# Performance work log

Hardware: AMD Instinct MI355X
Metric: run time of the kernel (lower is better)

The kernel has to match this reference:

```python
import jax, jax.numpy as jnp
import numpy as np

DIM = 1024
HIDDEN = 4096
NNZ = 262144
X_SHAPE = (2, 256, DIM)


def setup_inputs() -> dict:
    key = jax.random.key(0)
    ks = jax.random.split(key, 13)
    return {
        "x": jax.random.normal(ks[0], X_SHAPE, dtype=jnp.float32),
        "up_row": jax.random.randint(ks[1], (NNZ,), 0, HIDDEN),
        "up_col": jax.random.randint(ks[2], (NNZ,), 0, DIM),
        "up_val": jax.random.normal(ks[3], (NNZ,), dtype=jnp.float32),
        "up_bias": jax.random.normal(ks[4], (HIDDEN,), dtype=jnp.float32),
        "gate_row": jax.random.randint(ks[5], (NNZ,), 0, HIDDEN),
        "gate_col": jax.random.randint(ks[6], (NNZ,), 0, DIM),
        "gate_val": jax.random.normal(ks[7], (NNZ,), dtype=jnp.float32),
        "gate_bias": jax.random.normal(ks[8], (HIDDEN,), dtype=jnp.float32),
        "down_row": jax.random.randint(ks[9], (NNZ,), 0, DIM),
        "down_col": jax.random.randint(ks[10], (NNZ,), 0, HIDDEN),
        "down_val": jax.random.normal(ks[11], (NNZ,), dtype=jnp.float32),
        "down_bias": jax.random.normal(ks[12], (DIM,), dtype=jnp.float32),
    }


def _sparse_linear(x2d, row, col, val, bias, out_features):
    # x2d: [T, in_features]; COO: row -> out_features, col -> in_features
    weighted = x2d[:, col] * val  # [T, nnz], same expanded form as torch gather*mul
    # scatter_add over rows == segment_sum over the nnz axis
    out = jax.ops.segment_sum(weighted.T, row, num_segments=out_features).T  # [T, out]
    return out + bias


def reference(x, up_row, up_col, up_val, up_bias,
              gate_row, gate_col, gate_val, gate_bias,
              down_row, down_col, down_val, down_bias):
    in_shape = x.shape
    x2d = x.reshape(-1, DIM)  # [T, dim]
    up = _sparse_linear(x2d, up_row, up_col, up_val, up_bias, HIDDEN)
    gate = _sparse_linear(x2d, gate_row, gate_col, gate_val, gate_bias, HIDDEN)
    hidden = jax.nn.silu(up) * gate  # [T, hidden]
    down = _sparse_linear(hidden, down_row, down_col, down_val, down_bias, DIM)
    return (x2d + down).reshape(in_shape)
```

## Files before the change

### kernel.cpp

```cpp
#include <hip/hip_runtime.h>
#include <hip/hip_bf16.h>
#include <stdint.h>


#define DIM_    1024
#define HIDDEN_ 4096
#define NNZ_    262144
#define TTOK_   512
#define PADL_   12

typedef __attribute__((ext_vector_type(8))) short short8;
typedef __attribute__((ext_vector_type(4))) float float4v;

__device__ inline unsigned short f2bf(float f) {
    union { float f; unsigned int u; } c; c.f = f;
    unsigned int u = c.u;
    unsigned int r = u + 0x7fffu + ((u >> 16) & 1u);
    return (unsigned short)(r >> 16);
}

__device__ inline void async16(const unsigned short* g, unsigned short* l) {
    __builtin_amdgcn_global_load_lds(
        (const __attribute__((address_space(1))) unsigned int*)g,
        (__attribute__((address_space(3))) unsigned int*)l, 16, 0, 0);
}

#define PIPE_BAR(N)                                                         \
    __builtin_amdgcn_sched_barrier(0);                                      \
    asm volatile("s_waitcnt vmcnt(" #N ") lgkmcnt(0)" ::: "memory");        \
    __builtin_amdgcn_s_barrier();                                           \
    __builtin_amdgcn_sched_barrier(0);

#define XC_ ((TTOK_ * DIM_) / 4)

__global__ __launch_bounds__(256) void bin_prep_kernel(
    const int* __restrict__ ur, const int* __restrict__ uc, const float* __restrict__ uv,
    const int* __restrict__ gr, const int* __restrict__ gc, const float* __restrict__ gv,
    const int* __restrict__ dr, const int* __restrict__ dc, const float* __restrict__ dv,
    const float* __restrict__ x, const float* __restrict__ down_bias,
    unsigned int* __restrict__ bands, int* __restrict__ cnt,
    int* __restrict__ goc, uint2* __restrict__ gof,
    unsigned short* __restrict__ xb, float* __restrict__ out) {
    const int b = blockIdx.x;
    const int t = threadIdx.x;
    if (b >= 768) {
        const unsigned int u0 = (b - 768) * 1024 + t * 4;
        #pragma unroll
        for (int q = 0; q < 4; ++q) {
            const unsigned int id = u0 + q;
            if (id < XC_) {
                float4 v = ((const float4*)x)[id];
                ushort4 o;
                o.x = f2bf(v.x); o.y = f2bf(v.y); o.z = f2bf(v.z); o.w = f2bf(v.w);
                ((ushort4*)xb)[id] = o;
            } else {
                const unsigned int i = id - XC_;
                float4 v = ((const float4*)x)[i];
                const int d = (i * 4) & (DIM_ - 1);
                const float4 bb = *(const float4*)(down_bias + d);
                float4 o;
                o.x = v.x + bb.x; o.y = v.y + bb.y; o.z = v.z + bb.z; o.w = v.w + bb.w;
                ((float4*)out)[i] = o;
            }
        }
        return;
    }
    __shared__ unsigned int stage[256][PADL_];
    __shared__ int lcount[256];
    const int mat = b >> 8;
    const int chunk = b & 255;
    const int*   rs = (mat == 0) ? ur : (mat == 1) ? gr : dr;
    const int*   cs = (mat == 0) ? uc : (mat == 1) ? gc : dc;
    const float* vs = (mat == 0) ? uv : (mat == 1) ? gv : dv;
    const int shift = (mat == 2) ? 2 : 4;
    const int rmask = (mat == 2) ? 3 : 15;
    lcount[t] = 0;
    __syncthreads();

    const int base = chunk * 1024 + t * 4;
    int4   r4 = *(const int4*)(rs + base);
    int4   c4 = *(const int4*)(cs + base);
    float4 v4 = *(const float4*)(vs + base);
    int   rr[4] = {r4.x, r4.y, r4.z, r4.w};
    int   cc[4] = {c4.x, c4.y, c4.z, c4.w};
    float vv[4] = {v4.x, v4.y, v4.z, v4.w};
    #pragma unroll
    for (int j = 0; j < 4; ++j) {
        const int band = rr[j] >> shift;
        const unsigned int e = ((unsigned int)(rr[j] & rmask) << 28)
                             | ((unsigned int)cc[j] << 16)
                             | (unsigned int)f2bf(vv[j]);
        const int pos = atomicAdd(&lcount[band], 1);
        if (pos < PADL_) {
            stage[band][pos] = e;
        } else {
            const int op = atomicAdd(&goc[mat], 1);
            gof[mat * 4096 + op] = make_uint2((unsigned int)band, e);
        }
    }
    __syncthreads();
    unsigned int* seg = bands + ((unsigned int)(mat * 256 + t) * 256 + chunk) * PADL_;
    const uint4* sp = (const uint4*)&stage[t][0];
    *(uint4*)(seg)     = sp[0];
    *(uint4*)(seg + 4) = sp[1];
    *(uint4*)(seg + 8) = sp[2];
    cnt[(mat * 256 + t) * 256 + chunk] = lcount[t];
}

__global__ __launch_bounds__(512) void build_ug_kernel(
    const unsigned int* __restrict__ bands,
    const int* __restrict__ cnt,
    const int* __restrict__ goc, const uint2* __restrict__ gof,
    unsigned short* __restrict__ WUP,
    unsigned short* __restrict__ WGATE) {
    __shared__ float acc[8 * 1024];
    __shared__ int lcnt[256];
    const int b = blockIdx.x;
    const int t = threadIdx.x;
    const int mat = b >> 9;
    const int rem = b & 511;
    const int band = rem >> 1;
    const int hb = rem & 1;
    unsigned short* out = (mat ? WGATE : WUP) + (band * 16 + hb * 8) * 1024;
    const unsigned int rbase = hb * 8;

    for (int k = 0; k < 4; ++k)
        *(float4*)&acc[(k * 512 + t) * 4] = make_float4(0.f, 0.f, 0.f, 0.f);
    if (t < 256) lcnt[t] = cnt[(mat * 256 + band) * 256 + t];
    __syncthreads();

    const int chunk = t & 255;
    const int half = t >> 8;
    const unsigned int* seg = bands + ((unsigned int)(mat * 256 + band) * 256 + chunk) * PADL_;
    const int c = lcnt[chunk];

    if (half == 0) {
        uint4 q[3];
        const uint4* sp = (const uint4*)seg;
        #pragma unroll
        for (int i = 0; i < 3; ++i) q[i] = sp[i];
        const unsigned int* qq = (const unsigned int*)q;
        #pragma unroll
        for (int j = 0; j < PADL_; ++j) {
            const unsigned int e = qq[j];
            const unsigned int r2 = (e >> 28) - rbase;
            if (j < c && r2 < 8u)
                atomicAdd(&acc[r2 * 1024 + ((e >> 16) & 0xFFFu)],
                          __uint_as_float(e << 16));
        }
    } else {
        const int oc = goc[mat] < 4096 ? goc[mat] : 4096;
        for (int i = chunk; i < oc; i += 256) {
            uint2 oe = gof[mat * 4096 + i];
            if ((int)oe.x == band) {
                const unsigned int e = oe.y;
                const unsigned int r2 = (e >> 28) - rbase;
                if (r2 < 8u)
                    atomicAdd(&acc[r2 * 1024 + ((e >> 16) & 0xFFFu)],
                              __uint_as_float(e << 16));
            }
        }
    }
    __syncthreads();

    for (int k = 0; k < 4; ++k) {
        const int cc = (k * 512 + t) * 4;
        ushort4 o;
        o.x = f2bf(acc[cc]);     o.y = f2bf(acc[cc + 1]);
        o.z = f2bf(acc[cc + 2]); o.w = f2bf(acc[cc + 3]);
        *(ushort4*)(out + cc) = o;
    }
}

#define STAGE_UG(buf, k0)                                      \
    async16(gA + (k0),  sA_  + (buf) * 2048 + t * 8);          \
    async16(gBu + (k0), sBu_ + (buf) * 2048 + t * 8);          \
    async16(gBg + (k0), sBg_ + (buf) * 2048 + t * 8);

#define COMPUTE_UG(buf)                                                        \
    {                                                                          \
        const int kb = (buf) * 2048 + lkq * 8;                                 \
        short8 a[2], bu[2], bg[2];                                             \
        _Pragma("unroll")                                                      \
        for (int im = 0; im < 2; ++im)                                         \
            a[im] = *(const short8*)&sA_[kb + (wm + im * 16 + lr) * 32];       \
        _Pragma("unroll")                                                      \
        for (int in = 0; in < 2; ++in) {                                       \
            bu[in] = *(const short8*)&sBu_[kb + (wn + in * 16 + lr) * 32];     \
            bg[in] = *(const short8*)&sBg_[kb + (wn + in * 16 + lr) * 32];     \
        }                                                                      \
        _Pragma("unroll")                                                      \
        for (int im = 0; im < 2; ++im)                                         \
            _Pragma("unroll")                                                  \
            for (int in = 0; in < 2; ++in) {                                   \
                au[im][in] = __builtin_amdgcn_mfma_f32_16x16x32_bf16(          \
                    a[im], bu[in], au[im][in], 0, 0, 0);                       \
                ag[im][in] = __builtin_amdgcn_mfma_f32_16x16x32_bf16(          \
                    a[im], bg[in], ag[im][in], 0, 0, 0);                       \
            }                                                                  \
    }

__global__ __launch_bounds__(256) void fused_upgate_builddown_kernel(
    const unsigned short* __restrict__ xb,
    const unsigned short* __restrict__ wup,
    const unsigned short* __restrict__ wgate,
    const float* __restrict__ up_bias,
    const float* __restrict__ gate_bias,
    unsigned short* __restrict__ hid,
    const unsigned int* __restrict__ bands,
    const int* __restrict__ cnt,
    const int* __restrict__ goc, const uint2* __restrict__ gof,
    unsigned short* __restrict__ WDOWN) {
    __shared__ __align__(16) unsigned short smem_us[9 * 2048];
    const int b = blockIdx.x;
    const int t = threadIdx.x;

    if (b >= 512) {
        float* acc = (float*)smem_us;
        int*   lcnt = (int*)(smem_us + 16384);
        const int rem = b - 512;
        const int band = rem >> 1;
        const int hb = rem & 1;
        const unsigned int rbase = hb * 2;
        unsigned short* out = WDOWN + (band * 4 + hb * 2) * 4096;

        #pragma unroll
        for (int k = 0; k < 8; ++k)
            *(float4*)&acc[(k * 256 + t) * 4] = make_float4(0.f, 0.f, 0.f, 0.f);
        lcnt[t] = cnt[(2 * 256 + band) * 256 + t];
        __syncthreads();

        const unsigned int* seg = bands + ((unsigned int)(2 * 256 + band) * 256 + t) * PADL_;
        const int c = lcnt[t];
        uint4 q[3];
        const uint4* sp = (const uint4*)seg;
        #pragma unroll
        for (int i = 0; i < 3; ++i) q[i] = sp[i];
        const unsigned int* qq = (const unsigned int*)q;
        #pragma unroll
        for (int j = 0; j < PADL_; ++j) {
            const unsigned int e = qq[j];
            const unsigned int r2 = (e >> 28) - rbase;
            if (j < c && r2 < 2u)
                atomicAdd(&acc[r2 * 4096 + ((e >> 16) & 0xFFFu)],
                          __uint_as_float(e << 16));
        }
        const int oc = goc[2] < 4096 ? goc[2] : 4096;
        for (int i = t; i < oc; i += 256) {
            uint2 oe = gof[2 * 4096 + i];
            if ((int)oe.x == band) {
                const unsigned int e = oe.y;
                const unsigned int r2 = (e >> 28) - rbase;
                if (r2 < 2u)
                    atomicAdd(&acc[r2 * 4096 + ((e >> 16) & 0xFFFu)],
                              __uint_as_float(e << 16));
            }
        }
        __syncthreads();

        #pragma unroll
        for (int k = 0; k < 8; ++k) {
            const int cc = (k * 256 + t) * 4;
            ushort4 o;
            o.x = f2bf(acc[cc]);     o.y = f2bf(acc[cc + 1]);
            o.z = f2bf(acc[cc + 2]); o.w = f2bf(acc[cc + 3]);
            *(ushort4*)(out + cc) = o;
        }
        return;
    }

    unsigned short* sA_  = smem_us;
    unsigned short* sBu_ = smem_us + 3 * 2048;
    unsigned short* sBg_ = smem_us + 6 * 2048;
    const int n0 = (b & 63) * 64;
    const int m0 = (b >> 6) * 64;
    const int w = t >> 6, l = t & 63;
    const int wm = (w >> 1) * 32, wn = (w & 1) * 32;
    const int lr = l & 15, lkq = (l >> 4);

    float4v au[2][2], ag[2][2];
    for (int im = 0; im < 2; ++im)
        for (int in = 0; in < 2; ++in) {
            au[im][in] = float4v{0.f, 0.f, 0.f, 0.f};
            ag[im][in] = float4v{0.f, 0.f, 0.f, 0.f};
        }

    const int srow = t >> 2, scol = (t & 3) * 8;
    const unsigned short* gA  = xb    + (m0 + srow) * DIM_ + scol;
    const unsigned short* gBu = wup   + (n0 + srow) * DIM_ + scol;
    const unsigned short* gBg = wgate + (n0 + srow) * DIM_ + scol;

    STAGE_UG(0, 0);
    STAGE_UG(1, 32);
    int cur = 0;
    for (int k0 = 64; k0 < DIM_; k0 += 32) {
        PIPE_BAR(3);
        const int nn = cur == 0 ? 2 : cur - 1;
        STAGE_UG(nn, k0);
        COMPUTE_UG(cur);
        cur = cur == 2 ? 0 : cur + 1;
    }
    PIPE_BAR(3);
    COMPUTE_UG(cur);
    cur = cur == 2 ? 0 : cur + 1;
    PIPE_BAR(0);
    COMPUTE_UG(cur);

    for (int im = 0; im < 2; ++im) {
        for (int in = 0; in < 2; ++in) {
            const int n = n0 + wn + in * 16 + lr;
            const float ub = up_bias[n], gb = gate_bias[n];
            for (int r = 0; r < 4; ++r) {
                const int m = m0 + wm + im * 16 + lkq * 4 + r;
                const float u = au[im][in][r] + ub;
                const float g = ag[im][in][r] + gb;
                const float h = (u / (1.f + __expf(-u))) * g;
                hid[m * HIDDEN_ + n] = f2bf(h);
            }
        }
    }
}

#define STAGE_DN(buf, k0)                                      \
    async16(gA + (k0), sA + (buf) * 2048 + t * 8);             \
    async16(gB + (k0), sB + (buf) * 2048 + t * 8);

#define COMPUTE_DN(buf)                                                        \
    {                                                                          \
        const int kb = (buf) * 2048 + lkq * 8;                                 \
        short8 a[2], b2[2];                                                    \
        _Pragma("unroll")                                                      \
        for (int im = 0; im < 2; ++im)                                         \
            a[im] = *(const short8*)&sA[kb + (wm + im * 16 + lr) * 32];        \
        _Pragma("unroll")                                                      \
        for (int in = 0; in < 2; ++in)                                         \
            b2[in] = *(const short8*)&sB[kb + (wn + in * 16 + lr) * 32];       \
        _Pragma("unroll")                                                      \
        for (int im = 0; im < 2; ++im)                                         \
            _Pragma("unroll")                                                  \
            for (int in = 0; in < 2; ++in)                                     \
                acc[im][in] = __builtin_amdgcn_mfma_f32_16x16x32_bf16(         \
                    a[im], b2[in], acc[im][in], 0, 0, 0);                      \
    }

__global__ __launch_bounds__(256) void gemm_down_kernel(
    const unsigned short* __restrict__ hid,
    const unsigned short* __restrict__ wdown,
    float* __restrict__ out) {
    __shared__ __align__(16) unsigned short sA[3 * 2048];
    __shared__ __align__(16) unsigned short sB[3 * 2048];
    const int t = threadIdx.x;
    const int n0 = blockIdx.x * 64;
    const int m0 = blockIdx.y * 64;
    const int kb0 = blockIdx.z * 512;
    const int w = t >> 6, l = t & 63;
    const int wm = (w >> 1) * 32, wn = (w & 1) * 32;
    const int lr = l & 15, lkq = (l >> 4);

    float4v acc[2][2];
    for (int im = 0; im < 2; ++im)
        for (int in = 0; in < 2; ++in)
            acc[im][in] = float4v{0.f, 0.f, 0.f, 0.f};

    const int srow = t >> 2, scol = (t & 3) * 8;
    const unsigned short* gA = hid   + (m0 + srow) * HIDDEN_ + scol;
    const unsigned short* gB = wdown + (n0 + srow) * HIDDEN_ + scol;

    STAGE_DN(0, kb0);
    STAGE_DN(1, kb0 + 32);
    int cur = 0;
    for (int k0 = kb0 + 64; k0 < kb0 + 512; k0 += 32) {
        PIPE_BAR(2);
        const int nn = cur == 0 ? 2 : cur - 1;
        STAGE_DN(nn, k0);
        COMPUTE_DN(cur);
        cur = cur == 2 ? 0 : cur + 1;
    }
    PIPE_BAR(2);
    COMPUTE_DN(cur);
    cur = cur == 2 ? 0 : cur + 1;
    PIPE_BAR(0);
    COMPUTE_DN(cur);

    for (int im = 0; im < 2; ++im) {
        for (int in = 0; in < 2; ++in) {
            const int n = n0 + wn + in * 16 + lr;
            for (int r = 0; r < 4; ++r) {
                const int m = m0 + wm + im * 16 + lkq * 4 + r;
                atomicAdd(out + m * DIM_ + n, acc[im][in][r]);
            }
        }
    }
}

extern "C" void kernel_launch(void* const* d_in, const int* in_sizes, int n_in,
                              void* d_out, int out_size, void* d_ws, size_t ws_size,
                              hipStream_t stream) {
    const float* x         = (const float*)d_in[0];
    const int*   up_row    = (const int*)d_in[1];
    const int*   up_col    = (const int*)d_in[2];
    const float* up_val    = (const float*)d_in[3];
    const float* up_bias   = (const float*)d_in[4];
    const int*   gate_row  = (const int*)d_in[5];
    const int*   gate_col  = (const int*)d_in[6];
    const float* gate_val  = (const float*)d_in[7];
    const float* gate_bias = (const float*)d_in[8];
    const int*   down_row  = (const int*)d_in[9];
    const int*   down_col  = (const int*)d_in[10];
    const float* down_val  = (const float*)d_in[11];
    const float* down_bias = (const float*)d_in[12];
    float* out = (float*)d_out;

    unsigned char* ws = (unsigned char*)d_ws;
    unsigned short* WUP   = (unsigned short*)(ws);
    unsigned short* WGATE = (unsigned short*)(ws + (8u << 20));
    unsigned short* WDOWN = (unsigned short*)(ws + (16u << 20));
    unsigned short* XB    = (unsigned short*)(ws + (24u << 20));
    unsigned short* HID   = (unsigned short*)(ws + (25u << 20));
    unsigned int*   BANDS = (unsigned int*)(ws + (29u << 20));
    int*            CNT   = (int*)(ws + (66u << 20));
    int*            GOC   = (int*)(ws + (67u << 20));
    uint2*          GOF   = (uint2*)(ws + (67u << 20) + 64);

    hipMemsetAsync(GOC, 0, 3 * sizeof(int), stream);

    bin_prep_kernel<<<1024, 256, 0, stream>>>(
        up_row, up_col, up_val, gate_row, gate_col, gate_val,
        down_row, down_col, down_val, x, down_bias, BANDS, CNT, GOC, GOF, XB, out);

    build_ug_kernel<<<1024, 512, 0, stream>>>(BANDS, CNT, GOC, GOF, WUP, WGATE);

    fused_upgate_builddown_kernel<<<1024, 256, 0, stream>>>(
        XB, WUP, WGATE, up_bias, gate_bias, HID, BANDS, CNT, GOC, GOF, WDOWN);

    gemm_down_kernel<<<dim3(DIM_ / 64, TTOK_ / 64, 8), 256, 0, stream>>>(
        HID, WDOWN, out);
}
```

Measured before the change: 139.0 us.

## Use per-chunk overflow slots instead of global overflow counter; halve down split-K

```diff
diff --git a/kernel.cpp b/kernel.cpp
--- a/kernel.cpp
+++ b/kernel.cpp
@@ -8,6 +8,7 @@
 #define NNZ_    262144
 #define TTOK_   512
 #define PADL_   12
+#define OSLOTS_ 16
 
 typedef __attribute__((ext_vector_type(8))) short short8;
 typedef __attribute__((ext_vector_type(4))) float float4v;
@@ -39,7 +40,7 @@
     const int* __restrict__ dr, const int* __restrict__ dc, const float* __restrict__ dv,
     const float* __restrict__ x, const float* __restrict__ down_bias,
     unsigned int* __restrict__ bands, int* __restrict__ cnt,
-    int* __restrict__ goc, uint2* __restrict__ gof,
+    int* __restrict__ ocnt, uint2* __restrict__ gof,
     unsigned short* __restrict__ xb, float* __restrict__ out) {
     const int b = blockIdx.x;
     const int t = threadIdx.x;
@@ -67,6 +68,7 @@
     }
     __shared__ unsigned int stage[256][PADL_];
     __shared__ int lcount[256];
+    __shared__ int ocount;
     const int mat = b >> 8;
     const int chunk = b & 255;
     const int*   rs = (mat == 0) ? ur : (mat == 1) ? gr : dr;
@@ -75,6 +77,7 @@
     const int shift = (mat == 2) ? 2 : 4;
     const int rmask = (mat == 2) ? 3 : 15;
     lcount[t] = 0;
+    if (t == 0) ocount = 0;
     __syncthreads();
 
     const int base = chunk * 1024 + t * 4;
@@ -94,8 +97,10 @@
         if (pos < PADL_) {
             stage[band][pos] = e;
         } else {
-            const int op = atomicAdd(&goc[mat], 1);
-            gof[mat * 4096 + op] = make_uint2((unsigned int)band, e);
+            const int op = atomicAdd(&ocount, 1);
+            if (op < OSLOTS_)
+                gof[(mat * 256 + chunk) * OSLOTS_ + op] =
+                    make_uint2((unsigned int)band, e);
         }
     }
     __syncthreads();
@@ -105,12 +110,14 @@
     *(uint4*)(seg + 4) = sp[1];
     *(uint4*)(seg + 8) = sp[2];
     cnt[(mat * 256 + t) * 256 + chunk] = lcount[t];
+    if (t == 0)
+        ocnt[mat * 256 + chunk] = ocount < OSLOTS_ ? ocount : OSLOTS_;
 }
 
 __global__ __launch_bounds__(512) void build_ug_kernel(
     const unsigned int* __restrict__ bands,
     const int* __restrict__ cnt,
-    const int* __restrict__ goc, const uint2* __restrict__ gof,
+    const int* __restrict__ ocnt, const uint2* __restrict__ gof,
     unsigned short* __restrict__ WUP,
     unsigned short* __restrict__ WGATE) {
     __shared__ float acc[8 * 1024];
@@ -149,9 +156,10 @@
                           __uint_as_float(e << 16));
         }
     } else {
-        const int oc = goc[mat] < 4096 ? goc[mat] : 4096;
-        for (int i = chunk; i < oc; i += 256) {
-            uint2 oe = gof[mat * 4096 + i];
+        const int oc = ocnt[mat * 256 + chunk];
+        const uint2* og = gof + (mat * 256 + chunk) * OSLOTS_;
+        for (int i = 0; i < oc; ++i) {
+            uint2 oe = og[i];
             if ((int)oe.x == band) {
                 const unsigned int e = oe.y;
                 const unsigned int r2 = (e >> 28) - rbase;
@@ -209,7 +217,7 @@
     unsigned short* __restrict__ hid,
     const unsigned int* __restrict__ bands,
     const int* __restrict__ cnt,
-    const int* __restrict__ goc, const uint2* __restrict__ gof,
+    const int* __restrict__ ocnt, const uint2* __restrict__ gof,
     unsigned short* __restrict__ WDOWN) {
     __shared__ __align__(16) unsigned short smem_us[9 * 2048];
     const int b = blockIdx.x;
@@ -245,9 +253,10 @@
                 atomicAdd(&acc[r2 * 4096 + ((e >> 16) & 0xFFFu)],
                           __uint_as_float(e << 16));
         }
-        const int oc = goc[2] < 4096 ? goc[2] : 4096;
-        for (int i = t; i < oc; i += 256) {
-            uint2 oe = gof[2 * 4096 + i];
+        const int oc = ocnt[2 * 256 + t];
+        const uint2* og = gof + (2 * 256 + t) * OSLOTS_;
+        for (int i = 0; i < oc; ++i) {
+            uint2 oe = og[i];
             if ((int)oe.x == band) {
                 const unsigned int e = oe.y;
                 const unsigned int r2 = (e >> 28) - rbase;
@@ -352,7 +361,7 @@
     const int t = threadIdx.x;
     const int n0 = blockIdx.x * 64;
     const int m0 = blockIdx.y * 64;
-    const int kb0 = blockIdx.z * 512;
+    const int kb0 = blockIdx.z * 1024;
     const int w = t >> 6, l = t & 63;
     const int wm = (w >> 1) * 32, wn = (w & 1) * 32;
     const int lr = l & 15, lkq = (l >> 4);
@@ -369,7 +378,7 @@
     STAGE_DN(0, kb0);
     STAGE_DN(1, kb0 + 32);
     int cur = 0;
-    for (int k0 = kb0 + 64; k0 < kb0 + 512; k0 += 32) {
+    for (int k0 = kb0 + 64; k0 < kb0 + 1024; k0 += 32) {
         PIPE_BAR(2);
         const int nn = cur == 0 ? 2 : cur - 1;
         STAGE_DN(nn, k0);
@@ -419,20 +428,18 @@
     unsigned short* HID   = (unsigned short*)(ws + (25u << 20));
     unsigned int*   BANDS = (unsigned int*)(ws + (29u << 20));
     int*            CNT   = (int*)(ws + (66u << 20));
-    int*            GOC   = (int*)(ws + (67u << 20));
-    uint2*          GOF   = (uint2*)(ws + (67u << 20) + 64);
-
-    hipMemsetAsync(GOC, 0, 3 * sizeof(int), stream);
+    int*            OCNT  = (int*)(ws + (67u << 20));
+    uint2*          GOF   = (uint2*)(ws + (67u << 20) + 4096);
 
     bin_prep_kernel<<<1024, 256, 0, stream>>>(
         up_row, up_col, up_val, gate_row, gate_col, gate_val,
-        down_row, down_col, down_val, x, down_bias, BANDS, CNT, GOC, GOF, XB, out);
-
-    build_ug_kernel<<<1024, 512, 0, stream>>>(BANDS, CNT, GOC, GOF, WUP, WGATE);
+        down_row, down_col, down_val, x, down_bias, BANDS, CNT, OCNT, GOF, XB, out);
+
+    build_ug_kernel<<<1024, 512, 0, stream>>>(BANDS, CNT, OCNT, GOF, WUP, WGATE);
 
     fused_upgate_builddown_kernel<<<1024, 256, 0, stream>>>(
-        XB, WUP, WGATE, up_bias, gate_bias, HID, BANDS, CNT, GOC, GOF, WDOWN);
-
-    gemm_down_kernel<<<dim3(DIM_ / 64, TTOK_ / 64, 8), 256, 0, stream>>>(
+        XB, WUP, WGATE, up_bias, gate_bias, HID, BANDS, CNT, OCNT, GOF, WDOWN);
+
+    gemm_down_kernel<<<dim3(DIM_ / 64, TTOK_ / 64, 4), 256, 0, stream>>>(
         HID, WDOWN, out);
 }
```

New measurement: 134.2 us. -3.5%, faster.
